# Kernel tuning notes

Hardware: AMD Instinct MI355X
Metric: run time of the kernel (lower is better)

Reference implementation:

```python
import jax, jax.numpy as jnp
import numpy as np

LAM_CONSIST = 0.1
LAM_LR = 1.0
LAM_PAIR = 1.0


def _cubic(x, a=-0.75):
    # PyTorch bicubic kernel (a = -0.75)
    ax = jnp.abs(x)
    ax2 = ax * ax
    ax3 = ax2 * ax
    f1 = (a + 2.0) * ax3 - (a + 3.0) * ax2 + 1.0
    f2 = a * ax3 - 5.0 * a * ax2 + 8.0 * a * ax - 4.0 * a
    return jnp.where(ax <= 1.0, f1, jnp.where(ax < 2.0, f2, 0.0))


def _resize_matrix(in_size: int, out_size: int) -> jnp.ndarray:
    """Weight matrix [out_size, in_size] for antialiased bicubic resize
    (align_corners=False, antialias=True, border replicate) as in
    F.interpolate(..., mode='bicubic', antialias=True)."""
    scale = in_size / out_size
    s_aa = max(scale, 1.0)  # widen kernel when downscaling (antialias)
    support = 2.0 * s_aa
    ext = int(np.ceil(support)) + 1
    centers = (np.arange(out_size, dtype=np.float64) + 0.5) * scale - 0.5
    idx = np.arange(-ext, in_size + ext)
    dist = (idx[None, :] - centers[:, None]) / s_aa  # [out, in+2ext]
    w = _cubic(jnp.asarray(dist, dtype=jnp.float32))
    w = w / jnp.sum(w, axis=1, keepdims=True)  # torch normalizes window weights
    idx_c = np.clip(idx, 0, in_size - 1)  # clamp -> replicate border
    M = jnp.zeros((out_size, in_size), dtype=jnp.float32).at[:, idx_c].add(w)
    return M


def _resize_bicubic_aa(img: jnp.ndarray, th: int, tw: int) -> jnp.ndarray:
    # img: [B, C, H, W] -> [B, C, th, tw], separable resize via two matmuls
    _, _, h, w = img.shape
    Mh = _resize_matrix(h, th)  # [th, h]
    Mw = _resize_matrix(w, tw)  # [tw, w]
    return jnp.einsum('oh,bchw,pw->bcop', Mh, img, Mw)


def setup_inputs() -> dict:
    key = jax.random.key(0)
    k1, k2, k3 = jax.random.split(key, 3)
    pred_hr = jax.random.normal(k1, (32, 3, 512, 512), dtype=jnp.float32)
    target_hr = jax.random.normal(k2, (32, 3, 512, 512), dtype=jnp.float32)
    lr_ref = jax.random.normal(k3, (32, 3, 128, 128), dtype=jnp.float32)
    scale = jnp.full((32,), 4.0, dtype=jnp.float32)  # uniform -> static sizes
    return {"pred_hr": pred_hr, "target_hr": target_hr, "lr_ref": lr_ref, "scale": scale}


def reference(pred_hr, target_hr, lr_ref, scale):
    pix = jnp.mean(jnp.abs(pred_hr - target_hr))
    # project_scale(pred_hr, src=scale, dst=1): uniform scale=4 ->
    # target size == lr_ref spatial size (static, read from lr_ref shape)
    th, tw = lr_ref.shape[-2], lr_ref.shape[-1]
    pred_lr = _resize_bicubic_aa(pred_hr, th, tw)
    lr_term = jnp.mean(jnp.abs(pred_lr - lr_ref))
    pair_term = jnp.float32(0.0)  # pair_pred_hr / pair_scale are None
    consist = LAM_LR * lr_term + LAM_PAIR * pair_term
    total = pix + LAM_CONSIST * consist
    return (total, pix, consist, lr_term, pair_term)
```

## Files before the change

kernel.cpp:

```cpp
#include <hip/hip_runtime.h>

#define HW    512
#define OUTW  128
#define NIMG  96
#define N_HR  ((long long)NIMG*HW*HW)
#define N_LR  ((long long)NIMG*OUTW*OUTW)
#define NSLOT 256

__device__ __forceinline__ float cubic075(float x){
    float ax = fabsf(x);
    float ax2 = ax*ax, ax3 = ax2*ax;
    const float A = -0.75f;
    float f1 = (A+2.f)*ax3 - (A+3.f)*ax2 + 1.f;
    float f2 = A*ax3 - 5.f*A*ax2 + 8.f*A*ax - 4.f*A;
    return ax <= 1.f ? f1 : (ax < 2.f ? f2 : 0.f);
}

__device__ __forceinline__ void get_weights(float w[16]){
    float s = 0.f;
#pragma unroll
    for (int k = 0; k < 16; ++k){
        float d = ((float)k - 7.5f) * 0.25f;
        w[k] = cubic075(d);
        s += w[k];
    }
#pragma unroll
    for (int k = 0; k < 16; ++k) w[k] /= s;
}

__global__ void kinit(double* p){
    int i = blockIdx.x * blockDim.x + threadIdx.x;
    if (i < 2*NSLOT) p[i] = 0.0;
}

__global__ __launch_bounds__(256) void kmain(const float* __restrict__ pred,
                                             const float* __restrict__ tgt,
                                             const float* __restrict__ lr,
                                             double* __restrict__ p1,
                                             double* __restrict__ p2){
    const int img = blockIdx.x >> 3;
    const int o0  = (blockIdx.x & 7) << 4;
    const int s   = 4*o0 - 6;
    const int tid = threadIdx.x;
    const int w   = tid >> 6;
    const int l   = tid & 63;

    __shared__ float  ring[16][128];
    __shared__ double sred[8];

    float wt[16]; get_weights(wt);
    const float* P = pred + (size_t)img * HW * HW;
    const float* T = tgt  + (size_t)img * HW * HW;
    const float* L = lr   + (size_t)img * OUTW * OUTW;

    float pix_acc = 0.f, lr_acc = 0.f;

    int j = w;
    int hc = min(HW-1, max(0, s + j));
    const float4* rp = (const float4*)(P + (size_t)hc * HW);
    float4 a0 = rp[2*l], a1 = rp[2*l+1];

    for (int i = 0; i < 19; ++i){
        const int jcur = 4*i + w;
        const bool owned = (jcur >= 6 && jcur < 70);
        float4 b0, b1;
        if (owned){
            int hcc = min(HW-1, max(0, s + jcur));
            const float4* tp = (const float4*)(T + (size_t)hcc * HW);
            b0 = tp[2*l]; b1 = tp[2*l+1];
        }
        float p0=a0.x,p1v=a0.y,p2v=a0.z,p3=a0.w,p4=a1.x,p5=a1.y,p6=a1.z,p7=a1.w;

        if (i < 18){
            int jn = 4*(i+1) + w;
            int hn = min(HW-1, max(0, s + jn));
            const float4* rpn = (const float4*)(P + (size_t)hn * HW);
            a0 = rpn[2*l]; a1 = rpn[2*l+1];
        }

        if (owned){
            pix_acc += fabsf(p0-b0.x)+fabsf(p1v-b0.y)+fabsf(p2v-b0.z)+fabsf(p3-b0.w)
                     + fabsf(p4-b1.x)+fabsf(p5-b1.y)+fabsf(p6-b1.z)+fabsf(p7-b1.w);
        }

        float Lm6 = __shfl_up(p2v,1,64), Lm5 = __shfl_up(p3,1,64),
              Lm4 = __shfl_up(p4,1,64),  Lm3 = __shfl_up(p5,1,64),
              Lm2 = __shfl_up(p6,1,64),  Lm1 = __shfl_up(p7,1,64);
        float R8  = __shfl_down(p0,1,64), R9  = __shfl_down(p1v,1,64),
              R10 = __shfl_down(p2v,1,64),R11 = __shfl_down(p3,1,64),
              R12 = __shfl_down(p4,1,64), R13 = __shfl_down(p5,1,64);
        if (l == 0){ Lm6=p0; Lm5=p0; Lm4=p0; Lm3=p0; Lm2=p0; Lm1=p0; }
        if (l == 63){ R8=p7; R9=p7; R10=p7; R11=p7; R12=p7; R13=p7; }

        float w20[20] = {Lm6,Lm5,Lm4,Lm3,Lm2,Lm1,p0,p1v,p2v,p3,p4,p5,p6,p7,
                         R8,R9,R10,R11,R12,R13};
        float out0 = 0.f, out1 = 0.f;
#pragma unroll
        for (int k = 0; k < 16; ++k){
            out0 += wt[k]*w20[k];
            out1 += wt[k]*w20[k+4];
        }
        ring[jcur & 15][2*l]   = out0;
        ring[jcur & 15][2*l+1] = out1;

        __syncthreads();
        if (i >= 3 && tid < 128){
            const int q = i - 3;
            float acc = 0.f;
#pragma unroll
            for (int r = 0; r < 16; ++r)
                acc += wt[r] * ring[(4*q + r) & 15][tid];
            lr_acc += fabsf(acc - L[(size_t)(o0 + q) * OUTW + tid]);
        }
        __syncthreads();
    }

#pragma unroll
    for (int off = 32; off > 0; off >>= 1){
        pix_acc += __shfl_down(pix_acc, off, 64);
        lr_acc  += __shfl_down(lr_acc,  off, 64);
    }
    if (l == 0){ sred[w] = (double)pix_acc; sred[4+w] = (double)lr_acc; }
    __syncthreads();
    if (tid == 0){
        double S1 = sred[0]+sred[1]+sred[2]+sred[3];
        atomicAdd(&p1[blockIdx.x & (NSLOT-1)], S1);
    }
    if (tid == 64){
        double S2 = sred[4]+sred[5]+sred[6]+sred[7];
        atomicAdd(&p2[blockIdx.x & (NSLOT-1)], S2);
    }
}

__global__ __launch_bounds__(256) void k3(const double* __restrict__ p1,
                                          const double* __restrict__ p2,
                                          float* __restrict__ out){
    const int t = threadIdx.x;
    double v1 = p1[t], v2 = p2[t];
#pragma unroll
    for (int off = 32; off > 0; off >>= 1){
        v1 += __shfl_down(v1, off, 64);
        v2 += __shfl_down(v2, off, 64);
    }
    __shared__ double s1[4], s2[4];
    const int lane = t & 63, wid = t >> 6;
    if (lane == 0){ s1[wid] = v1; s2[wid] = v2; }
    __syncthreads();
    if (t == 0){
        double S1 = s1[0]+s1[1]+s1[2]+s1[3];
        double S2 = s2[0]+s2[1]+s2[2]+s2[3];
        float pix     = (float)(S1 / (double)N_HR);
        float lr_term = (float)(S2 / (double)N_LR);
        float pair    = 0.f;
        float consist = 1.0f * lr_term + 1.0f * pair;
        float total   = pix + 0.1f * consist;
        out[0] = total; out[1] = pix; out[2] = consist; out[3] = lr_term; out[4] = pair;
    }
}

extern "C" void kernel_launch(void* const* d_in, const int* in_sizes, int n_in,
                              void* d_out, int out_size, void* d_ws, size_t ws_size,
                              hipStream_t stream){
    const float* pred = (const float*)d_in[0];
    const float* tgt  = (const float*)d_in[1];
    const float* lrr  = (const float*)d_in[2];
    float* out = (float*)d_out;

    double* p1 = (double*)d_ws;
    double* p2 = p1 + NSLOT;

    kinit<<<2, 256, 0, stream>>>(p1);
    kmain<<<NIMG*8, 256, 0, stream>>>(pred, tgt, lrr, p1, p2);
    k3<<<1, 256, 0, stream>>>(p1, p2, out);
}
```

Measured before the change: 232.7 us.

## Give each wavefront its own output rows and drop shared-memory ring and barriers

```diff
diff --git a/kernel.cpp b/kernel.cpp
--- a/kernel.cpp
+++ b/kernel.cpp
@@ -5,7 +5,7 @@
 #define NIMG  96
 #define N_HR  ((long long)NIMG*HW*HW)
 #define N_LR  ((long long)NIMG*OUTW*OUTW)
-#define NSLOT 256
+#define NPART (NIMG*32)
 
 __device__ __forceinline__ float cubic075(float x){
     float ax = fabsf(x);
@@ -28,59 +28,53 @@
     for (int k = 0; k < 16; ++k) w[k] /= s;
 }
 
-__global__ void kinit(double* p){
-    int i = blockIdx.x * blockDim.x + threadIdx.x;
-    if (i < 2*NSLOT) p[i] = 0.0;
-}
-
 __global__ __launch_bounds__(256) void kmain(const float* __restrict__ pred,
                                              const float* __restrict__ tgt,
                                              const float* __restrict__ lr,
-                                             double* __restrict__ p1,
-                                             double* __restrict__ p2){
+                                             double* __restrict__ part){
     const int img = blockIdx.x >> 3;
-    const int o0  = (blockIdx.x & 7) << 4;
-    const int s   = 4*o0 - 6;
     const int tid = threadIdx.x;
     const int w   = tid >> 6;
     const int l   = tid & 63;
-
-    __shared__ float  ring[16][128];
-    __shared__ double sred[8];
+    const int gw  = ((blockIdx.x & 7) << 2) + w;
+    const int o0  = gw << 2;
+    const int s   = (gw << 4) - 6;
 
     float wt[16]; get_weights(wt);
-    const float* P = pred + (size_t)img * HW * HW;
-    const float* T = tgt  + (size_t)img * HW * HW;
-    const float* L = lr   + (size_t)img * OUTW * OUTW;
+    const float* P = pred + (size_t)img * (HW*HW);
+    const float* T = tgt  + (size_t)img * (HW*HW);
+    const float* L = lr   + (size_t)img * (OUTW*OUTW);
 
+    float acc[4][2] = {{0.f,0.f},{0.f,0.f},{0.f,0.f},{0.f,0.f}};
     float pix_acc = 0.f, lr_acc = 0.f;
 
-    int j = w;
-    int hc = min(HW-1, max(0, s + j));
-    const float4* rp = (const float4*)(P + (size_t)hc * HW);
-    float4 a0 = rp[2*l], a1 = rp[2*l+1];
+    int r0 = min(HW-1, max(0, s + 0));
+    int r1 = min(HW-1, max(0, s + 1));
+    const float4* rp0 = (const float4*)(P + (size_t)r0 * HW);
+    const float4* rp1 = (const float4*)(P + (size_t)r1 * HW);
+    float4 c0 = rp0[2*l], c1 = rp0[2*l+1];
+    float4 n0 = rp1[2*l], n1 = rp1[2*l+1];
+    float4 tc0, tc1, tn0, tn1;
 
-    for (int i = 0; i < 19; ++i){
-        const int jcur = 4*i + w;
-        const bool owned = (jcur >= 6 && jcur < 70);
-        float4 b0, b1;
-        if (owned){
-            int hcc = min(HW-1, max(0, s + jcur));
-            const float4* tp = (const float4*)(T + (size_t)hcc * HW);
-            b0 = tp[2*l]; b1 = tp[2*l+1];
+#pragma unroll 4
+    for (int i = 0; i < 28; ++i){
+        float4 f0, f1, tf0, tf1;
+        if (i < 26){
+            int rn = min(HW-1, max(0, s + i + 2));
+            const float4* rp = (const float4*)(P + (size_t)rn * HW);
+            f0 = rp[2*l]; f1 = rp[2*l+1];
         }
-        float p0=a0.x,p1v=a0.y,p2v=a0.z,p3=a0.w,p4=a1.x,p5=a1.y,p6=a1.z,p7=a1.w;
-
-        if (i < 18){
-            int jn = 4*(i+1) + w;
-            int hn = min(HW-1, max(0, s + jn));
-            const float4* rpn = (const float4*)(P + (size_t)hn * HW);
-            a0 = rpn[2*l]; a1 = rpn[2*l+1];
+        if (i + 2 >= 6 && i + 2 < 22){
+            const float4* tp = (const float4*)(T + (size_t)(s + i + 2) * HW);
+            tf0 = tp[2*l]; tf1 = tp[2*l+1];
         }
 
-        if (owned){
-            pix_acc += fabsf(p0-b0.x)+fabsf(p1v-b0.y)+fabsf(p2v-b0.z)+fabsf(p3-b0.w)
-                     + fabsf(p4-b1.x)+fabsf(p5-b1.y)+fabsf(p6-b1.z)+fabsf(p7-b1.w);
+        const float p0=c0.x,p1v=c0.y,p2v=c0.z,p3=c0.w,
+                    p4=c1.x,p5=c1.y,p6=c1.z,p7=c1.w;
+
+        if (i >= 6 && i < 22){
+            pix_acc += fabsf(p0-tc0.x)+fabsf(p1v-tc0.y)+fabsf(p2v-tc0.z)+fabsf(p3-tc0.w)
+                     + fabsf(p4-tc1.x)+fabsf(p5-tc1.y)+fabsf(p6-tc1.z)+fabsf(p7-tc1.w);
         }
 
         float Lm6 = __shfl_up(p2v,1,64), Lm5 = __shfl_up(p3,1,64),
@@ -94,25 +88,30 @@
 
         float w20[20] = {Lm6,Lm5,Lm4,Lm3,Lm2,Lm1,p0,p1v,p2v,p3,p4,p5,p6,p7,
                          R8,R9,R10,R11,R12,R13};
-        float out0 = 0.f, out1 = 0.f;
+        float h0 = 0.f, h1 = 0.f;
 #pragma unroll
         for (int k = 0; k < 16; ++k){
-            out0 += wt[k]*w20[k];
-            out1 += wt[k]*w20[k+4];
+            h0 += wt[k]*w20[k];
+            h1 += wt[k]*w20[k+4];
         }
-        ring[jcur & 15][2*l]   = out0;
-        ring[jcur & 15][2*l+1] = out1;
 
-        __syncthreads();
-        if (i >= 3 && tid < 128){
-            const int q = i - 3;
-            float acc = 0.f;
 #pragma unroll
-            for (int r = 0; r < 16; ++r)
-                acc += wt[r] * ring[(4*q + r) & 15][tid];
-            lr_acc += fabsf(acc - L[(size_t)(o0 + q) * OUTW + tid]);
+        for (int q = 0; q < 4; ++q){
+            int k = i - 4*q;
+            if (k >= 0 && k < 16){
+                acc[q][0] += wt[k]*h0;
+                acc[q][1] += wt[k]*h1;
+            }
         }
-        __syncthreads();
+
+        c0=n0; c1=n1; n0=f0; n1=f1;
+        tc0=tn0; tc1=tn1; tn0=tf0; tn1=tf1;
+    }
+
+#pragma unroll
+    for (int q = 0; q < 4; ++q){
+        const float2 lv = *(const float2*)(L + (size_t)(o0+q)*OUTW + 2*l);
+        lr_acc += fabsf(acc[q][0]-lv.x) + fabsf(acc[q][1]-lv.y);
     }
 
 #pragma unroll
@@ -120,23 +119,21 @@
         pix_acc += __shfl_down(pix_acc, off, 64);
         lr_acc  += __shfl_down(lr_acc,  off, 64);
     }
-    if (l == 0){ sred[w] = (double)pix_acc; sred[4+w] = (double)lr_acc; }
-    __syncthreads();
-    if (tid == 0){
-        double S1 = sred[0]+sred[1]+sred[2]+sred[3];
-        atomicAdd(&p1[blockIdx.x & (NSLOT-1)], S1);
-    }
-    if (tid == 64){
-        double S2 = sred[4]+sred[5]+sred[6]+sred[7];
-        atomicAdd(&p2[blockIdx.x & (NSLOT-1)], S2);
+    if (l == 0){
+        const int slot = (blockIdx.x << 2) + w;
+        part[slot]         = (double)pix_acc;
+        part[NPART + slot] = (double)lr_acc;
     }
 }
 
-__global__ __launch_bounds__(256) void k3(const double* __restrict__ p1,
-                                          const double* __restrict__ p2,
+__global__ __launch_bounds__(256) void k3(const double* __restrict__ part,
                                           float* __restrict__ out){
     const int t = threadIdx.x;
-    double v1 = p1[t], v2 = p2[t];
+    double v1 = 0.0, v2 = 0.0;
+    for (int i = t; i < NPART; i += 256){
+        v1 += part[i];
+        v2 += part[NPART + i];
+    }
 #pragma unroll
     for (int off = 32; off > 0; off >>= 1){
         v1 += __shfl_down(v1, off, 64);
@@ -166,10 +163,8 @@
     const float* lrr  = (const float*)d_in[2];
     float* out = (float*)d_out;
 
-    double* p1 = (double*)d_ws;
-    double* p2 = p1 + NSLOT;
+    double* part = (double*)d_ws;
 
-    kinit<<<2, 256, 0, stream>>>(p1);
-    kmain<<<NIMG*8, 256, 0, stream>>>(pred, tgt, lrr, p1, p2);
-    k3<<<1, 256, 0, stream>>>(p1, p2, out);
+    kmain<<<NIMG*8, 256, 0, stream>>>(pred, tgt, lrr, part);
+    k3<<<1, 256, 0, stream>>>(part, out);
 }
```

Result: no change. 229.5 us (-1.3%).
